# Optimization experiments

Measured on AMD Instinct MI355X. Metric: run time of the kernel, lower is better.

Reference implementation:

```python
import jax, jax.numpy as jnp
import numpy as np

ACT_DIM = 768
DICT_SIZE = 16384
K = 64
BATCH = 2048


def setup_inputs() -> dict:
    key = jax.random.key(0)
    k_x, k_w, k_be = jax.random.split(key, 3)
    x = jax.random.normal(k_x, (BATCH, ACT_DIM), dtype=jnp.float32)
    # encoder weight [dict_size, act_dim]; decoder initialized as encoder.T with unit-norm columns
    W_enc = jax.random.normal(k_w, (DICT_SIZE, ACT_DIM), dtype=jnp.float32) * 0.02
    b_enc = jnp.zeros((DICT_SIZE,), dtype=jnp.float32)
    W_dec = W_enc.T  # [act_dim, dict_size]
    eps = jnp.finfo(jnp.float32).eps
    W_dec = W_dec / (jnp.linalg.norm(W_dec, axis=0, keepdims=True) + eps)
    b_dec = jnp.zeros((ACT_DIM,), dtype=jnp.float32)
    return {"x": x, "W_enc": W_enc, "b_enc": b_enc, "W_dec": W_dec, "b_dec": b_dec}


def reference(x, W_enc, b_enc, W_dec, b_dec):
    B = x.shape[0]
    # encode: linear on (x - b_dec), relu
    post_relu_BF = jax.nn.relu((x - b_dec) @ W_enc.T + b_enc)  # [B, F]
    flat = post_relu_BF.reshape(-1)  # [B*F]
    # global batch top-k: keep k*B largest activations across the whole batch
    vals, idx = jax.lax.top_k(flat, K * B)
    encoded_flat = jnp.zeros_like(flat).at[idx].set(vals)
    encoded_BF = encoded_flat.reshape(post_relu_BF.shape)
    # decode
    x_hat_BD = encoded_BF @ W_dec.T + b_dec  # [B, D]
    return x_hat_BD
```

## Files before the change

### kernel.cpp

```cpp
#include <hip/hip_runtime.h>
#include <stdint.h>

#define BATCH   2048
#define DIM     768
#define FEAT    16384
#define KSEL    64
#define KB_SEL  (BATCH * KSEL)
#define N_TOT   (BATCH * FEAT)
#define NX4     (BATCH * DIM / 4)
#define NW4     (FEAT * DIM / 4)

#define GBM 128
#define GBN 128
#define GBK 32
#define AROW   24
#define APLANE 3088

#define SAMP_ROWS 128
#define SAMP_N    12288
#define CCAP      262144
#define TIE_CAP   1024
#define LSTAGE    2048
#define FG        8
#define FBLK      (CCAP / (FG * 4))

#define PREP_BLKS 4096
#define WT_BLKS   (512 * 24)

#define SL_T32    0
#define SL_NC     1
#define SL_DEF    2
#define SL_NTIE   3
#define SL_WIN    4
#define SL_S0     16

typedef __attribute__((ext_vector_type(8))) __bf16 bf16x8;
typedef __attribute__((ext_vector_type(4))) float  f32x4;
typedef unsigned long long u64;

__device__ __forceinline__ unsigned short bf16r(float v)
{
    unsigned u = __float_as_uint(v);
    u += 0x7FFFu + ((u >> 16) & 1u);
    return (unsigned short)(u >> 16);
}

__device__ __forceinline__ unsigned wave_append(unsigned* counter, bool pred)
{
    unsigned long long m = __ballot(pred);
    if (m == 0ull) return 0xFFFFFFFFu;
    const int lane = threadIdx.x & 63;
    const int leader = __ffsll((unsigned long long)m) - 1;
    unsigned base = 0;
    if (lane == leader) base = atomicAdd(counter, (unsigned)__popcll(m));
    base = __shfl(base, leader, 64);
    if (!pred) return 0xFFFFFFFFu;
    return base + (unsigned)__popcll(m & ((1ull << lane) - 1ull));
}

__global__ __launch_bounds__(256) void sae19_prepwt(const float* __restrict__ x,
                                                    const float* __restrict__ Wenc,
                                                    const float* __restrict__ Wdec,
                                                    const float* __restrict__ bdec,
                                                    unsigned short* __restrict__ xb,
                                                    unsigned short* __restrict__ wb,
                                                    unsigned short* __restrict__ Wtb)
{
    __shared__ float t[32][33];
    if (blockIdx.x < PREP_BLKS) {
        const int tot = NX4 + NW4;
        for (int i = blockIdx.x * 256 + threadIdx.x; i < tot; i += PREP_BLKS * 256) {
            if (i < NX4) {
                const int e = i * 4;
                const int d = e % DIM;
                float4 v  = *(const float4*)(x + e);
                float4 dv = *(const float4*)(bdec + d);
                uint2 p;
                p.x = (unsigned)bf16r(v.x - dv.x) | ((unsigned)bf16r(v.y - dv.y) << 16);
                p.y = (unsigned)bf16r(v.z - dv.z) | ((unsigned)bf16r(v.w - dv.w) << 16);
                *(uint2*)(xb + e) = p;
            } else {
                const int e = (i - NX4) * 4;
                float4 v = *(const float4*)(Wenc + e);
                uint2 p;
                p.x = (unsigned)bf16r(v.x) | ((unsigned)bf16r(v.y) << 16);
                p.y = (unsigned)bf16r(v.z) | ((unsigned)bf16r(v.w) << 16);
                *(uint2*)(wb + e) = p;
            }
        }
    } else {
        const int wtb = blockIdx.x - PREP_BLKS;
        const int f0 = (wtb % 512) * 32;
        const int d0 = (wtb / 512) * 32;
        const int tx = threadIdx.x & 31;
        const int ty = threadIdx.x >> 5;
#pragma unroll
        for (int i = 0; i < 4; ++i)
            t[ty + i * 8][tx] = Wdec[(size_t)(d0 + ty + i * 8) * FEAT + f0 + tx];
        __syncthreads();
#pragma unroll
        for (int i = 0; i < 4; ++i)
            Wtb[(size_t)(f0 + ty + i * 8) * DIM + d0 + tx] = bf16r(t[tx][ty + i * 8]);
    }
}

__global__ __launch_bounds__(256) void sae19_sgemm(const unsigned short* __restrict__ xb,
                                                   const unsigned short* __restrict__ wb,
                                                   const float* __restrict__ benc,
                                                   unsigned* __restrict__ hist)
{
    __shared__ unsigned short Als[4 * APLANE];
    __shared__ unsigned short Bls[4 * APLANE];
    __shared__ unsigned h[8192];

    const int tid  = threadIdx.x;
    for (int i = tid; i < 8192; i += 256) h[i] = 0u;
    const int row0 = 0;
    const int col0 = blockIdx.x * GBN;
    const int wid  = tid >> 6;
    const int lane = tid & 63;
    const int wr = wid >> 1;
    const int wc = wid & 1;
    const int fr = lane & 15;
    const int kg = lane >> 4;

    f32x4 acc[4][4];
#pragma unroll
    for (int i = 0; i < 4; ++i)
#pragma unroll
        for (int j = 0; j < 4; ++j) acc[i][j] = (f32x4){0.f, 0.f, 0.f, 0.f};

    for (int kt = 0; kt < DIM; kt += GBK) {
#pragma unroll
        for (int i = 0; i < 4; ++i) {
            const int idx = i * 256 + tid;
            const int r   = idx >> 3;
            const int kq  = (idx & 7) * 4;
            const int g   = kq >> 3;
            const int k0  = kq & 7;
            *(uint2*)&Als[g * APLANE + r * AROW + k0] =
                *(const uint2*)(xb + (size_t)(row0 + r) * DIM + kt + kq);
            *(uint2*)&Bls[g * APLANE + r * AROW + k0] =
                *(const uint2*)(wb + (size_t)(col0 + r) * DIM + kt + kq);
        }
        __syncthreads();

        bf16x8 afr[4], bfr[4];
#pragma unroll
        for (int mi = 0; mi < 4; ++mi)
            afr[mi] = *(const bf16x8*)&Als[kg * APLANE + (wr * 64 + mi * 16 + fr) * AROW];
#pragma unroll
        for (int ni = 0; ni < 4; ++ni)
            bfr[ni] = *(const bf16x8*)&Bls[kg * APLANE + (wc * 64 + ni * 16 + fr) * AROW];
#pragma unroll
        for (int mi = 0; mi < 4; ++mi)
#pragma unroll
            for (int ni = 0; ni < 4; ++ni)
                acc[mi][ni] = __builtin_amdgcn_mfma_f32_16x16x32_bf16(
                    afr[mi], bfr[ni], acc[mi][ni], 0, 0, 0);
        __syncthreads();
    }

#pragma unroll
    for (int ni = 0; ni < 4; ++ni) {
        const int col = col0 + wc * 64 + ni * 16 + fr;
        const float be = benc[col];
#pragma unroll
        for (int mi = 0; mi < 4; ++mi) {
#pragma unroll
            for (int j = 0; j < 4; ++j) {
                unsigned short bits = bf16r(fmaxf(acc[mi][ni][j] + be, 0.f));
                if (bits) atomicAdd(&h[bits >> 2], 1u);
            }
        }
    }
    __syncthreads();
    for (int i = tid; i < 8192; i += 256) {
        unsigned c = h[i];
        if (c) atomicAdd(&hist[i], c);
    }
}

__global__ __launch_bounds__(1024) void sae19_selb(const unsigned* __restrict__ hist,
                                                   unsigned* sl)
{
    __shared__ unsigned s[1024];
    const int t = threadIdx.x;
    const int C = 8;
    const unsigned N = (unsigned)SAMP_N;
    const int lo = t * C;
    unsigned S = 0;
    for (int i = 0; i < C; ++i) S += hist[lo + i];
    s[t] = S;
    __syncthreads();
    for (int off = 1; off < 1024; off <<= 1) {
        unsigned v = (t + off < 1024) ? s[t + off] : 0u;
        __syncthreads();
        s[t] += v;
        __syncthreads();
    }
    const unsigned incl  = s[t];
    const unsigned above = incl - S;
    if (above < N && N <= incl) {
        unsigned cum = above;
        for (int i = lo + C - 1; i >= lo; --i) {
            cum += hist[i];
            if (cum >= N) { sl[SL_T32] = (unsigned)i << 2; break; }
        }
    }
}

__global__ __launch_bounds__(256) void sae19_gemm(const unsigned short* __restrict__ xb,
                                                  const unsigned short* __restrict__ wb,
                                                  const float* __restrict__ benc,
                                                  unsigned* __restrict__ sl,
                                                  int* __restrict__ cand_raw)
{
    __shared__ unsigned short Als[4 * APLANE];
    __shared__ unsigned short Bls[4 * APLANE];
    __shared__ unsigned lcnt;
    __shared__ unsigned gbase;

    const int tid  = threadIdx.x;
    if (tid == 0) lcnt = 0;
    const int row0 = blockIdx.y * GBM;
    const int col0 = blockIdx.x * GBN;
    const int wid  = tid >> 6;
    const int lane = tid & 63;
    const int wr = wid >> 1;
    const int wc = wid & 1;
    const int fr = lane & 15;
    const int kg = lane >> 4;

    f32x4 acc[4][4];
#pragma unroll
    for (int i = 0; i < 4; ++i)
#pragma unroll
        for (int j = 0; j < 4; ++j) acc[i][j] = (f32x4){0.f, 0.f, 0.f, 0.f};

    for (int kt = 0; kt < DIM; kt += GBK) {
#pragma unroll
        for (int i = 0; i < 4; ++i) {
            const int idx = i * 256 + tid;
            const int r   = idx >> 3;
            const int kq  = (idx & 7) * 4;
            const int g   = kq >> 3;
            const int k0  = kq & 7;
            *(uint2*)&Als[g * APLANE + r * AROW + k0] =
                *(const uint2*)(xb + (size_t)(row0 + r) * DIM + kt + kq);
            *(uint2*)&Bls[g * APLANE + r * AROW + k0] =
                *(const uint2*)(wb + (size_t)(col0 + r) * DIM + kt + kq);
        }
        __syncthreads();

        bf16x8 afr[4], bfr[4];
#pragma unroll
        for (int mi = 0; mi < 4; ++mi)
            afr[mi] = *(const bf16x8*)&Als[kg * APLANE + (wr * 64 + mi * 16 + fr) * AROW];
#pragma unroll
        for (int ni = 0; ni < 4; ++ni)
            bfr[ni] = *(const bf16x8*)&Bls[kg * APLANE + (wc * 64 + ni * 16 + fr) * AROW];
#pragma unroll
        for (int mi = 0; mi < 4; ++mi)
#pragma unroll
            for (int ni = 0; ni < 4; ++ni)
                acc[mi][ni] = __builtin_amdgcn_mfma_f32_16x16x32_bf16(
                    afr[mi], bfr[ni], acc[mi][ni], 0, 0, 0);
        __syncthreads();
    }

    int* loc = (int*)Als;
    const unsigned T = sl[SL_T32];
#pragma unroll
    for (int ni = 0; ni < 4; ++ni) {
        const int col = col0 + wc * 64 + ni * 16 + fr;
        const float be = benc[col];
#pragma unroll
        for (int mi = 0; mi < 4; ++mi) {
            const int rbase = row0 + wr * 64 + mi * 16 + kg * 4;
#pragma unroll
            for (int j = 0; j < 4; ++j) {
                unsigned short bits = bf16r(fmaxf(acc[mi][ni][j] + be, 0.f));
                if ((unsigned)bits >= T) {
                    unsigned p = atomicAdd(&lcnt, 1u);
                    if (p < (unsigned)LSTAGE) loc[p] = (rbase + j) * FEAT + col;
                }
            }
        }
    }
    __syncthreads();
    unsigned n = lcnt;
    if (n > (unsigned)LSTAGE) n = (unsigned)LSTAGE;
    if (tid == 0) gbase = atomicAdd(&sl[SL_NC], n);
    __syncthreads();
    const unsigned base = gbase;
    for (unsigned k = tid; k < n; k += 256) {
        unsigned dst = base + k;
        if (dst < (unsigned)CCAP) cand_raw[dst] = loc[k];
    }
}

__global__ __launch_bounds__(256) void sae19_fhist(const int* __restrict__ cand_raw,
                                                   const unsigned* __restrict__ sl,
                                                   unsigned* __restrict__ fhist)
{
    __shared__ unsigned h[16384];
    const int t = threadIdx.x;
    for (int i = t; i < 16384; i += 256) h[i] = 0u;
    __syncthreads();
    unsigned NC = sl[SL_NC];
    if (NC > (unsigned)CCAP) NC = (unsigned)CCAP;
    for (int i = blockIdx.x * 256 + t; i < (int)NC; i += gridDim.x * 256)
        atomicAdd(&h[cand_raw[i] & (FEAT - 1)], 1u);
    __syncthreads();
    for (int i = t; i < 16384; i += 256) {
        unsigned c = h[i];
        if (c) atomicAdd(&fhist[i], c);
    }
}

__global__ __launch_bounds__(1024) void sae19_fscan(const unsigned* __restrict__ fhist,
                                                    unsigned* __restrict__ fofs)
{
    __shared__ unsigned s[1024];
    const int t = threadIdx.x;
    unsigned c[16];
    unsigned sum = 0;
#pragma unroll
    for (int j = 0; j < 16; ++j) { c[j] = fhist[t * 16 + j]; sum += c[j]; }
    s[t] = sum;
    __syncthreads();
    for (int off = 1; off < 1024; off <<= 1) {
        unsigned v = (t >= off) ? s[t - off] : 0u;
        __syncthreads();
        s[t] += v;
        __syncthreads();
    }
    unsigned run = s[t] - sum;
#pragma unroll
    for (int j = 0; j < 16; ++j) { fofs[t * 16 + j] = run; run += c[j]; }
}

__global__ __launch_bounds__(256) void sae19_fscat(const int* __restrict__ cand_raw,
                                                   const unsigned* __restrict__ sl,
                                                   const unsigned* __restrict__ fofs,
                                                   unsigned* __restrict__ fcur,
                                                   int* __restrict__ cand_flat)
{
    unsigned NC = sl[SL_NC];
    if (NC > (unsigned)CCAP) NC = (unsigned)CCAP;
    for (int i = blockIdx.x * 256 + threadIdx.x; i < (int)NC; i += gridDim.x * 256) {
        int flat = cand_raw[i];
        int f = flat & (FEAT - 1);
        unsigned p = atomicAdd(&fcur[f], 1u);
        unsigned dst = fofs[f] + p;
        if (dst < (unsigned)CCAP) cand_flat[dst] = flat;
    }
}

__global__ __launch_bounds__(256) void sae19_feval(const float* __restrict__ x,
                                                   const float* __restrict__ Wenc,
                                                   const float* __restrict__ benc,
                                                   const float* __restrict__ bdec,
                                                   const unsigned* __restrict__ sl,
                                                   const int* __restrict__ cand_flat,
                                                   u64* __restrict__ cand_key)
{
    unsigned NC = sl[SL_NC];
    if (NC > (unsigned)CCAP) NC = (unsigned)CCAP;
    const int lane = threadIdx.x & 63;
    const int b = blockIdx.x;
    const int lb = (b & 7) * (FBLK / 8) + (b >> 3);
    const int wid = lb * 4 + (threadIdx.x >> 6);
    const int c0 = wid * FG;
    if (c0 >= (int)NC) return;

    float bd[12], wv[12];
#pragma unroll
    for (int j = 0; j < 12; ++j) bd[j] = bdec[lane + j * 64];
    int fprev = -1;

    for (int g = 0; g < FG; ++g) {
        const int c = c0 + g;
        if (c >= (int)NC) break;
        const int flat = cand_flat[c];
        const int bb = flat >> 14;
        const int f  = flat & (FEAT - 1);
        if (f != fprev) {
            const float* wr = Wenc + (size_t)f * DIM;
#pragma unroll
            for (int j = 0; j < 12; ++j) wv[j] = wr[lane + j * 64];
            fprev = f;
        }
        const float* xr = x + (size_t)bb * DIM;
        double p = 0.0;
#pragma unroll
        for (int j = 0; j < 12; ++j)
            p = fma((double)xr[lane + j * 64] - (double)bd[j], (double)wv[j], p);
#pragma unroll
        for (int o = 32; o > 0; o >>= 1) p += __shfl_xor(p, o, 64);
        if (lane == 0) {
            p += (double)benc[f];
            if (p < 0.0) p = 0.0;
            cand_key[c] = (u64)__double_as_longlong(p);
        }
    }
}

__global__ __launch_bounds__(256) void sae19_hist64(const u64* __restrict__ cand_key,
                                                    const unsigned* __restrict__ sl,
                                                    unsigned* __restrict__ hist,
                                                    int pass)
{
    __shared__ unsigned h[16384];
    const int t = threadIdx.x;
    for (int i = t; i < 16384; i += 256) h[i] = 0u;
    __syncthreads();

    unsigned NC = sl[SL_NC];
    if (NC > (unsigned)CCAP) NC = (unsigned)CCAP;
    u64 pref = 0;
    for (int i = 0; i < pass; ++i) pref = (pref << 14) | (u64)sl[SL_S0 + i];
    const int chk_sh = 64 - 14 * pass;
    const int bkt_sh = 50 - 14 * pass;

    for (int i = blockIdx.x * 256 + t; i < (int)NC; i += gridDim.x * 256) {
        u64 key = cand_key[i];
        if (pass > 0 && (key >> chk_sh) != pref) continue;
        atomicAdd(&h[(unsigned)(key >> bkt_sh) & 0x3FFFu], 1u);
    }
    __syncthreads();
    for (int i = t; i < 16384; i += 256) {
        unsigned c = h[i];
        if (c) atomicAdd(&hist[i], c);
    }
}

__global__ __launch_bounds__(1024) void sae19_sel14(const unsigned* __restrict__ hist,
                                                    unsigned* sl, int pass)
{
    __shared__ unsigned s[1024];
    const int t = threadIdx.x;
    const int C = 16;
    const unsigned N = (pass == 0) ? (unsigned)KB_SEL : sl[SL_S0 + 4 + pass - 1];
    const int lo = t * C;
    unsigned S = 0;
    for (int i = 0; i < C; ++i) S += hist[lo + i];
    s[t] = S;
    __syncthreads();
    for (int off = 1; off < 1024; off <<= 1) {
        unsigned v = (t + off < 1024) ? s[t + off] : 0u;
        __syncthreads();
        s[t] += v;
        __syncthreads();
    }
    const unsigned incl  = s[t];
    const unsigned above = incl - S;
    if (above < N && N <= incl) {
        unsigned cum = above;
        for (int i = lo + C - 1; i >= lo; --i) {
            cum += hist[i];
            if (cum >= N) {
                sl[SL_S0 + pass]     = (unsigned)i;
                sl[SL_S0 + 4 + pass] = N - (cum - hist[i]);
                break;
            }
        }
    }
}

__global__ __launch_bounds__(256) void sae19_maxb(const u64* __restrict__ cand_key,
                                                  const unsigned* __restrict__ sl,
                                                  u64* __restrict__ mx)
{
    unsigned NC = sl[SL_NC];
    if (NC > (unsigned)CCAP) NC = (unsigned)CCAP;
    const u64 Tsh1 = ((u64)sl[SL_S0 + 0] << 28) | ((u64)sl[SL_S0 + 1] << 14) |
                     (u64)sl[SL_S0 + 2];
    u64 m = 0;
    for (int i = blockIdx.x * 256 + threadIdx.x; i < (int)NC; i += gridDim.x * 256) {
        u64 k = cand_key[i];
        if ((k >> 22) < Tsh1 && k > m) m = k;
    }
#pragma unroll
    for (int o = 32; o > 0; o >>= 1) {
        u64 o2 = __shfl_xor(m, o, 64);
        if (o2 > m) m = o2;
    }
    if ((threadIdx.x & 63) == 0 && m) atomicMax((unsigned long long*)mx, m);
}

__global__ __launch_bounds__(256) void sae19_class(const u64* __restrict__ cand_key,
                                                   const int* __restrict__ cand_flat,
                                                   const u64* __restrict__ mx,
                                                   unsigned* __restrict__ sl,
                                                   unsigned* __restrict__ row_cnt,
                                                   int* __restrict__ sel_flat,
                                                   float* __restrict__ sel_val,
                                                   int* __restrict__ tie_flat,
                                                   u64* __restrict__ tie_key)
{
    unsigned NC = sl[SL_NC];
    if (NC > (unsigned)CCAP) NC = (unsigned)CCAP;
    const u64 Tsh1 = ((u64)sl[SL_S0 + 0] << 28) | ((u64)sl[SL_S0 + 1] << 14) |
                     (u64)sl[SL_S0 + 2];
    const u64 Tsh2 = mx[0] >> 22;
    const int c = blockIdx.x * 256 + threadIdx.x;
    const bool active = (c < (int)NC);
    u64 key = 0;
    int flat = 0;
    u64 keysh = 0;
    if (active) {
        key = cand_key[c];
        keysh = key >> 22;
        flat = cand_flat[c];
    }
    const bool selp = active && (keysh > Tsh1);
    unsigned p = wave_append(&sl[SL_DEF], selp);
    if (selp && p < (unsigned)KB_SEL) {
        sel_flat[p] = flat;
        sel_val[p]  = (float)__longlong_as_double((long long)key);
        atomicAdd(&row_cnt[flat >> 14], 1u);
    }
    const bool tiep = active && !selp && (keysh == Tsh2);
    unsigned q = wave_append(&sl[SL_NTIE], tiep);
    if (tiep && q < (unsigned)TIE_CAP) { tie_flat[q] = flat; tie_key[q] = key; }
}

__global__ __launch_bounds__(256) void sae19_ties(const int* __restrict__ tie_flat,
                                                  const u64* __restrict__ tie_key,
                                                  unsigned* __restrict__ sl,
                                                  int* __restrict__ sel_flat,
                                                  float* __restrict__ sel_val,
                                                  unsigned* __restrict__ row_cnt)
{
    unsigned R = sl[SL_NTIE];
    if (R > (unsigned)TIE_CAP) R = (unsigned)TIE_CAP;
    const unsigned REM = sl[SL_S0 + 6];
    const unsigned D = sl[SL_DEF];
    const int c = blockIdx.x * blockDim.x + threadIdx.x;
    if (c >= (int)R) return;
    const int ic = tie_flat[c];
    unsigned rank = 0;
    for (int j = 0; j < (int)R; ++j)
        if (tie_flat[j] < ic) ++rank;
    if (rank < REM) {
        unsigned p = D + atomicAdd(&sl[SL_WIN], 1u);
        if (p < (unsigned)KB_SEL) {
            sel_flat[p] = ic;
            sel_val[p]  = (float)__longlong_as_double((long long)tie_key[c]);
            atomicAdd(&row_cnt[ic >> 14], 1u);
        }
    }
}

__global__ __launch_bounds__(256) void sae19_scan(const unsigned* __restrict__ row_cnt,
                                                  unsigned* __restrict__ row_ofs)
{
    __shared__ unsigned s[256];
    const int t = threadIdx.x;
    unsigned c[8];
    unsigned sum = 0;
#pragma unroll
    for (int j = 0; j < 8; ++j) { c[j] = row_cnt[t * 8 + j]; sum += c[j]; }
    s[t] = sum;
    __syncthreads();
    for (int off = 1; off < 256; off <<= 1) {
        unsigned v = (t >= off) ? s[t - off] : 0u;
        __syncthreads();
        s[t] += v;
        __syncthreads();
    }
    unsigned run = s[t] - sum;
#pragma unroll
    for (int j = 0; j < 8; ++j) { row_ofs[t * 8 + j] = run; run += c[j]; }
    if (t == 255) row_ofs[2048] = run;
}

__global__ void sae19_scatter(const int* __restrict__ sel_flat,
                              const float* __restrict__ sel_val,
                              const unsigned* __restrict__ row_ofs,
                              unsigned* __restrict__ cursor,
                              int* __restrict__ gf, float* __restrict__ gv)
{
    int e = blockIdx.x * blockDim.x + threadIdx.x;
    if (e >= KB_SEL) return;
    int flat = sel_flat[e];
    int b = flat >> 14;
    unsigned p = atomicAdd(&cursor[b], 1u);
    unsigned dst = row_ofs[b] + p;
    if (dst < (unsigned)KB_SEL) {
        gf[dst] = flat & (FEAT - 1);
        gv[dst] = sel_val[e];
    }
}

__global__ __launch_bounds__(256) void sae19_decode(const int* __restrict__ gf,
                                                    const float* __restrict__ gv,
                                                    const unsigned* __restrict__ row_ofs,
                                                    const unsigned short* __restrict__ Wtb,
                                                    const float* __restrict__ bdec,
                                                    float* __restrict__ out)
{
    const int b = blockIdx.x;
    const int t = threadIdx.x;
    float a0 = 0.f, a1 = 0.f, a2 = 0.f;
    const unsigned s = row_ofs[b];
    const unsigned e = row_ofs[b + 1];
    for (unsigned i = s; i < e; ++i) {
        const int f   = gf[i];
        const float v = gv[i];
        const unsigned short* w = Wtb + (size_t)f * DIM;
        a0 = fmaf(v, __uint_as_float((unsigned)w[t]       << 16), a0);
        a1 = fmaf(v, __uint_as_float((unsigned)w[t + 256] << 16), a1);
        a2 = fmaf(v, __uint_as_float((unsigned)w[t + 512] << 16), a2);
    }
    out[(size_t)b * DIM + t]       = a0 + bdec[t];
    out[(size_t)b * DIM + t + 256] = a1 + bdec[t + 256];
    out[(size_t)b * DIM + t + 512] = a2 + bdec[t + 512];
}

extern "C" void kernel_launch(void* const* d_in, const int* in_sizes, int n_in,
                              void* d_out, int out_size, void* d_ws, size_t ws_size,
                              hipStream_t stream)
{
    (void)in_sizes; (void)n_in; (void)out_size;
    const float* x    = (const float*)d_in[0];
    const float* Wenc = (const float*)d_in[1];
    const float* benc = (const float*)d_in[2];
    const float* Wdec = (const float*)d_in[3];
    const float* bdec = (const float*)d_in[4];
    float* out = (float*)d_out;

    char* ws = (char*)d_ws;
    size_t off = 0;
    unsigned short* Wtb = (unsigned short*)(ws + off);     off += (size_t)FEAT * DIM * 2;
    unsigned short* xb  = (unsigned short*)(ws + off);     off += (size_t)BATCH * DIM * 2;
    unsigned short* wb  = (unsigned short*)(ws + off);     off += (size_t)FEAT * DIM * 2;
    u64*      cand_key  = (u64*)(ws + off);                off += (size_t)CCAP * 8;
    int*      cand_raw  = (int*)(ws + off);                off += (size_t)CCAP * 4;
    int*      cand_flat = (int*)(ws + off);                off += (size_t)CCAP * 4;
    int*      tie_flat  = (int*)(ws + off);                off += (size_t)TIE_CAP * 4;
    u64*      tie_key   = (u64*)(ws + off);                off += (size_t)TIE_CAP * 8;
    unsigned* row_ofs   = (unsigned*)(ws + off);           off += 2052 * 4;
    unsigned* fofs      = (unsigned*)(ws + off);           off += 16384 * 4;
    char* zstart = ws + off;
    int*      sel_flat  = (int*)(ws + off);                off += (size_t)KB_SEL * 4;
    float*    sel_val   = (float*)(ws + off);              off += (size_t)KB_SEL * 4;
    int*      gf        = (int*)(ws + off);                off += (size_t)KB_SEL * 4;
    float*    gv        = (float*)(ws + off);              off += (size_t)KB_SEL * 4;
    unsigned* hist1     = (unsigned*)(ws + off);           off += 8192 * 4;
    unsigned* h64       = (unsigned*)(ws + off);           off += 3 * 16384 * 4;
    unsigned* fhist     = (unsigned*)(ws + off);           off += 16384 * 4;
    unsigned* fcur      = (unsigned*)(ws + off);           off += 16384 * 4;
    unsigned* row_cnt   = (unsigned*)(ws + off);           off += 2048 * 4;
    unsigned* cursor    = (unsigned*)(ws + off);           off += 2048 * 4;
    u64*      mx        = (u64*)(ws + off);                off += 8;
    unsigned* sl        = (unsigned*)(ws + off);           off += 256;
    const size_t zbytes = (size_t)((ws + off) - zstart);
    if (ws_size < off) return;

    hipMemsetAsync(zstart, 0, zbytes, stream);

    sae19_prepwt<<<PREP_BLKS + WT_BLKS, 256, 0, stream>>>(x, Wenc, Wdec, bdec, xb, wb, Wtb);

    sae19_sgemm<<<dim3(FEAT / GBN, 1), 256, 0, stream>>>(xb, wb, benc, hist1);
    sae19_selb<<<1, 1024, 0, stream>>>(hist1, sl);

    sae19_gemm<<<dim3(FEAT / GBN, BATCH / GBM), 256, 0, stream>>>(xb, wb, benc, sl, cand_raw);

    sae19_fhist<<<256, 256, 0, stream>>>(cand_raw, sl, fhist);
    sae19_fscan<<<1, 1024, 0, stream>>>(fhist, fofs);
    sae19_fscat<<<256, 256, 0, stream>>>(cand_raw, sl, fofs, fcur, cand_flat);
    sae19_feval<<<FBLK, 256, 0, stream>>>(x, Wenc, benc, bdec, sl, cand_flat, cand_key);

    for (int p = 0; p < 3; ++p) {
        sae19_hist64<<<256, 256, 0, stream>>>(cand_key, sl, h64 + p * 16384, p);
        sae19_sel14<<<1, 1024, 0, stream>>>(h64 + p * 16384, sl, p);
    }
    sae19_maxb<<<256, 256, 0, stream>>>(cand_key, sl, mx);

    sae19_class<<<(CCAP + 255) / 256, 256, 0, stream>>>(cand_key, cand_flat, mx, sl, row_cnt,
                                                        sel_flat, sel_val, tie_flat, tie_key);
    sae19_ties<<<TIE_CAP / 256, 256, 0, stream>>>(tie_flat, tie_key, sl,
                                                  sel_flat, sel_val, row_cnt);

    sae19_scan<<<1, 256, 0, stream>>>(row_cnt, row_ofs);
    sae19_scatter<<<(KB_SEL + 255) / 256, 256, 0, stream>>>(sel_flat, sel_val, row_ofs, cursor, gf, gv);
    sae19_decode<<<BATCH, 256, 0, stream>>>(gf, gv, row_ofs, Wtb, bdec, out);
}
```

Before: 432.0 us.

## Lower sample quota, use float threshold compare in gemm, dual-accumulate decode

Result: no change. 426.3 us (-1.3%).

```diff
diff --git a/kernel.cpp b/kernel.cpp
--- a/kernel.cpp
+++ b/kernel.cpp
@@ -17,7 +17,7 @@
 #define APLANE 3088
 
 #define SAMP_ROWS 128
-#define SAMP_N    12288
+#define SAMP_N    10752
 #define CCAP      262144
 #define TIE_CAP   1024
 #define LSTAGE    2048
@@ -32,6 +32,7 @@
 #define SL_DEF    2
 #define SL_NTIE   3
 #define SL_WIN    4
+#define SL_THRF   8
 #define SL_S0     16
 
 typedef __attribute__((ext_vector_type(8))) __bf16 bf16x8;
@@ -58,7 +59,7 @@
     return base + (unsigned)__popcll(m & ((1ull << lane) - 1ull));
 }
 
-__global__ __launch_bounds__(256) void sae19_prepwt(const float* __restrict__ x,
+__global__ __launch_bounds__(256) void sae20_prepwt(const float* __restrict__ x,
                                                     const float* __restrict__ Wenc,
                                                     const float* __restrict__ Wdec,
                                                     const float* __restrict__ bdec,
@@ -104,7 +105,7 @@
     }
 }
 
-__global__ __launch_bounds__(256) void sae19_sgemm(const unsigned short* __restrict__ xb,
+__global__ __launch_bounds__(256) void sae20_sgemm(const unsigned short* __restrict__ xb,
                                                    const unsigned short* __restrict__ wb,
                                                    const float* __restrict__ benc,
                                                    unsigned* __restrict__ hist)
@@ -181,7 +182,7 @@
     }
 }
 
-__global__ __launch_bounds__(1024) void sae19_selb(const unsigned* __restrict__ hist,
+__global__ __launch_bounds__(1024) void sae20_selb(const unsigned* __restrict__ hist,
                                                    unsigned* sl)
 {
     __shared__ unsigned s[1024];
@@ -205,12 +206,17 @@
         unsigned cum = above;
         for (int i = lo + C - 1; i >= lo; --i) {
             cum += hist[i];
-            if (cum >= N) { sl[SL_T32] = (unsigned)i << 2; break; }
-        }
-    }
-}
-
-__global__ __launch_bounds__(256) void sae19_gemm(const unsigned short* __restrict__ xb,
+            if (cum >= N) {
+                sl[SL_T32] = (unsigned)i << 2;
+                unsigned tb = (i > 0) ? ((unsigned)(i - 1) << 2) : 0u;
+                sl[SL_THRF] = tb << 16;
+                break;
+            }
+        }
+    }
+}
+
+__global__ __launch_bounds__(256) void sae20_gemm(const unsigned short* __restrict__ xb,
                                                   const unsigned short* __restrict__ wb,
                                                   const float* __restrict__ benc,
                                                   unsigned* __restrict__ sl,
@@ -270,7 +276,7 @@
     }
 
     int* loc = (int*)Als;
-    const unsigned T = sl[SL_T32];
+    const float thr = __uint_as_float(sl[SL_THRF]);
 #pragma unroll
     for (int ni = 0; ni < 4; ++ni) {
         const int col = col0 + wc * 64 + ni * 16 + fr;
@@ -280,8 +286,7 @@
             const int rbase = row0 + wr * 64 + mi * 16 + kg * 4;
 #pragma unroll
             for (int j = 0; j < 4; ++j) {
-                unsigned short bits = bf16r(fmaxf(acc[mi][ni][j] + be, 0.f));
-                if ((unsigned)bits >= T) {
+                if (acc[mi][ni][j] + be > thr) {
                     unsigned p = atomicAdd(&lcnt, 1u);
                     if (p < (unsigned)LSTAGE) loc[p] = (rbase + j) * FEAT + col;
                 }
@@ -300,7 +305,7 @@
     }
 }
 
-__global__ __launch_bounds__(256) void sae19_fhist(const int* __restrict__ cand_raw,
+__global__ __launch_bounds__(256) void sae20_fhist(const int* __restrict__ cand_raw,
                                                    const unsigned* __restrict__ sl,
                                                    unsigned* __restrict__ fhist)
 {
@@ -319,7 +324,7 @@
     }
 }
 
-__global__ __launch_bounds__(1024) void sae19_fscan(const unsigned* __restrict__ fhist,
+__global__ __launch_bounds__(1024) void sae20_fscan(const unsigned* __restrict__ fhist,
                                                     unsigned* __restrict__ fofs)
 {
     __shared__ unsigned s[1024];
@@ -341,7 +346,7 @@
     for (int j = 0; j < 16; ++j) { fofs[t * 16 + j] = run; run += c[j]; }
 }
 
-__global__ __launch_bounds__(256) void sae19_fscat(const int* __restrict__ cand_raw,
+__global__ __launch_bounds__(256) void sae20_fscat(const int* __restrict__ cand_raw,
                                                    const unsigned* __restrict__ sl,
                                                    const unsigned* __restrict__ fofs,
                                                    unsigned* __restrict__ fcur,
@@ -358,7 +363,7 @@
     }
 }
 
-__global__ __launch_bounds__(256) void sae19_feval(const float* __restrict__ x,
+__global__ __launch_bounds__(256) void sae20_feval(const float* __restrict__ x,
                                                    const float* __restrict__ Wenc,
                                                    const float* __restrict__ benc,
                                                    const float* __restrict__ bdec,
@@ -407,7 +412,7 @@
     }
 }
 
-__global__ __launch_bounds__(256) void sae19_hist64(const u64* __restrict__ cand_key,
+__global__ __launch_bounds__(256) void sae20_hist64(const u64* __restrict__ cand_key,
                                                     const unsigned* __restrict__ sl,
                                                     unsigned* __restrict__ hist,
                                                     int pass)
@@ -436,7 +441,7 @@
     }
 }
 
-__global__ __launch_bounds__(1024) void sae19_sel14(const unsigned* __restrict__ hist,
+__global__ __launch_bounds__(1024) void sae20_sel14(const unsigned* __restrict__ hist,
                                                     unsigned* sl, int pass)
 {
     __shared__ unsigned s[1024];
@@ -469,7 +474,7 @@
     }
 }
 
-__global__ __launch_bounds__(256) void sae19_maxb(const u64* __restrict__ cand_key,
+__global__ __launch_bounds__(256) void sae20_maxb(const u64* __restrict__ cand_key,
                                                   const unsigned* __restrict__ sl,
                                                   u64* __restrict__ mx)
 {
@@ -490,7 +495,7 @@
     if ((threadIdx.x & 63) == 0 && m) atomicMax((unsigned long long*)mx, m);
 }
 
-__global__ __launch_bounds__(256) void sae19_class(const u64* __restrict__ cand_key,
+__global__ __launch_bounds__(256) void sae20_class(const u64* __restrict__ cand_key,
                                                    const int* __restrict__ cand_flat,
                                                    const u64* __restrict__ mx,
                                                    unsigned* __restrict__ sl,
@@ -527,7 +532,7 @@
     if (tiep && q < (unsigned)TIE_CAP) { tie_flat[q] = flat; tie_key[q] = key; }
 }
 
-__global__ __launch_bounds__(256) void sae19_ties(const int* __restrict__ tie_flat,
+__global__ __launch_bounds__(256) void sae20_ties(const int* __restrict__ tie_flat,
                                                   const u64* __restrict__ tie_key,
                                                   unsigned* __restrict__ sl,
                                                   int* __restrict__ sel_flat,
@@ -554,7 +559,7 @@
     }
 }
 
-__global__ __launch_bounds__(256) void sae19_scan(const unsigned* __restrict__ row_cnt,
+__global__ __launch_bounds__(256) void sae20_scan(const unsigned* __restrict__ row_cnt,
                                                   unsigned* __restrict__ row_ofs)
 {
     __shared__ unsigned s[256];
@@ -577,7 +582,7 @@
     if (t == 255) row_ofs[2048] = run;
 }
 
-__global__ void sae19_scatter(const int* __restrict__ sel_flat,
+__global__ void sae20_scatter(const int* __restrict__ sel_flat,
                               const float* __restrict__ sel_val,
                               const unsigned* __restrict__ row_ofs,
                               unsigned* __restrict__ cursor,
@@ -595,7 +600,7 @@
     }
 }
 
-__global__ __launch_bounds__(256) void sae19_decode(const int* __restrict__ gf,
+__global__ __launch_bounds__(256) void sae20_decode(const int* __restrict__ gf,
                                                     const float* __restrict__ gv,
                                                     const unsigned* __restrict__ row_ofs,
                                                     const unsigned short* __restrict__ Wtb,
@@ -605,19 +610,35 @@
     const int b = blockIdx.x;
     const int t = threadIdx.x;
     float a0 = 0.f, a1 = 0.f, a2 = 0.f;
+    float c0 = 0.f, c1 = 0.f, c2 = 0.f;
     const unsigned s = row_ofs[b];
     const unsigned e = row_ofs[b + 1];
-    for (unsigned i = s; i < e; ++i) {
-        const int f   = gf[i];
-        const float v = gv[i];
-        const unsigned short* w = Wtb + (size_t)f * DIM;
-        a0 = fmaf(v, __uint_as_float((unsigned)w[t]       << 16), a0);
-        a1 = fmaf(v, __uint_as_float((unsigned)w[t + 256] << 16), a1);
-        a2 = fmaf(v, __uint_as_float((unsigned)w[t + 512] << 16), a2);
-    }
-    out[(size_t)b * DIM + t]       = a0 + bdec[t];
-    out[(size_t)b * DIM + t + 256] = a1 + bdec[t + 256];
-    out[(size_t)b * DIM + t + 512] = a2 + bdec[t + 512];
+    unsigned i = s;
+    for (; i + 1 < e; i += 2) {
+        const int f0 = gf[i];
+        const int f1 = gf[i + 1];
+        const float v0 = gv[i];
+        const float v1 = gv[i + 1];
+        const unsigned short* w0 = Wtb + (size_t)f0 * DIM;
+        const unsigned short* w1 = Wtb + (size_t)f1 * DIM;
+        a0 = fmaf(v0, __uint_as_float((unsigned)w0[t]       << 16), a0);
+        c0 = fmaf(v1, __uint_as_float((unsigned)w1[t]       << 16), c0);
+        a1 = fmaf(v0, __uint_as_float((unsigned)w0[t + 256] << 16), a1);
+        c1 = fmaf(v1, __uint_as_float((unsigned)w1[t + 256] << 16), c1);
+        a2 = fmaf(v0, __uint_as_float((unsigned)w0[t + 512] << 16), a2);
+        c2 = fmaf(v1, __uint_as_float((unsigned)w1[t + 512] << 16), c2);
+    }
+    if (i < e) {
+        const int f0 = gf[i];
+        const float v0 = gv[i];
+        const unsigned short* w0 = Wtb + (size_t)f0 * DIM;
+        a0 = fmaf(v0, __uint_as_float((unsigned)w0[t]       << 16), a0);
+        a1 = fmaf(v0, __uint_as_float((unsigned)w0[t + 256] << 16), a1);
+        a2 = fmaf(v0, __uint_as_float((unsigned)w0[t + 512] << 16), a2);
+    }
+    out[(size_t)b * DIM + t]       = (a0 + c0) + bdec[t];
+    out[(size_t)b * DIM + t + 256] = (a1 + c1) + bdec[t + 256];
+    out[(size_t)b * DIM + t + 512] = (a2 + c2) + bdec[t + 512];
 }
 
 extern "C" void kernel_launch(void* const* d_in, const int* in_sizes, int n_in,
@@ -662,30 +683,30 @@
 
     hipMemsetAsync(zstart, 0, zbytes, stream);
 
-    sae19_prepwt<<<PREP_BLKS + WT_BLKS, 256, 0, stream>>>(x, Wenc, Wdec, bdec, xb, wb, Wtb);
-
-    sae19_sgemm<<<dim3(FEAT / GBN, 1), 256, 0, stream>>>(xb, wb, benc, hist1);
-    sae19_selb<<<1, 1024, 0, stream>>>(hist1, sl);
-
-    sae19_gemm<<<dim3(FEAT / GBN, BATCH / GBM), 256, 0, stream>>>(xb, wb, benc, sl, cand_raw);
-
-    sae19_fhist<<<256, 256, 0, stream>>>(cand_raw, sl, fhist);
-    sae19_fscan<<<1, 1024, 0, stream>>>(fhist, fofs);
-    sae19_fscat<<<256, 256, 0, stream>>>(cand_raw, sl, fofs, fcur, cand_flat);
-    sae19_feval<<<FBLK, 256, 0, stream>>>(x, Wenc, benc, bdec, sl, cand_flat, cand_key);
+    sae20_prepwt<<<PREP_BLKS + WT_BLKS, 256, 0, stream>>>(x, Wenc, Wdec, bdec, xb, wb, Wtb);
+
+    sae20_sgemm<<<dim3(FEAT / GBN, 1), 256, 0, stream>>>(xb, wb, benc, hist1);
+    sae20_selb<<<1, 1024, 0, stream>>>(hist1, sl);
+
+    sae20_gemm<<<dim3(FEAT / GBN, BATCH / GBM), 256, 0, stream>>>(xb, wb, benc, sl, cand_raw);
+
+    sae20_fhist<<<256, 256, 0, stream>>>(cand_raw, sl, fhist);
+    sae20_fscan<<<1, 1024, 0, stream>>>(fhist, fofs);
+    sae20_fscat<<<256, 256, 0, stream>>>(cand_raw, sl, fofs, fcur, cand_flat);
+    sae20_feval<<<FBLK, 256, 0, stream>>>(x, Wenc, benc, bdec, sl, cand_flat, cand_key);
 
     for (int p = 0; p < 3; ++p) {
-        sae19_hist64<<<256, 256, 0, stream>>>(cand_key, sl, h64 + p * 16384, p);
-        sae19_sel14<<<1, 1024, 0, stream>>>(h64 + p * 16384, sl, p);
-    }
-    sae19_maxb<<<256, 256, 0, stream>>>(cand_key, sl, mx);
-
-    sae19_class<<<(CCAP + 255) / 256, 256, 0, stream>>>(cand_key, cand_flat, mx, sl, row_cnt,
+        sae20_hist64<<<256, 256, 0, stream>>>(cand_key, sl, h64 + p * 16384, p);
+        sae20_sel14<<<1, 1024, 0, stream>>>(h64 + p * 16384, sl, p);
+    }
+    sae20_maxb<<<256, 256, 0, stream>>>(cand_key, sl, mx);
+
+    sae20_class<<<(CCAP + 255) / 256, 256, 0, stream>>>(cand_key, cand_flat, mx, sl, row_cnt,
                                                         sel_flat, sel_val, tie_flat, tie_key);
-    sae19_ties<<<TIE_CAP / 256, 256, 0, stream>>>(tie_flat, tie_key, sl,
+    sae20_ties<<<TIE_CAP / 256, 256, 0, stream>>>(tie_flat, tie_key, sl,
                                                   sel_flat, sel_val, row_cnt);
 
-    sae19_scan<<<1, 256, 0, stream>>>(row_cnt, row_ofs);
-    sae19_scatter<<<(KB_SEL + 255) / 256, 256, 0, stream>>>(sel_flat, sel_val, row_ofs, cursor, gf, gv);
-    sae19_decode<<<BATCH, 256, 0, stream>>>(gf, gv, row_ofs, Wtb, bdec, out);
-}
+    sae20_scan<<<1, 256, 0, stream>>>(row_cnt, row_ofs);
+    sae20_scatter<<<(KB_SEL + 255) / 256, 256, 0, stream>>>(sel_flat, sel_val, row_ofs, cursor, gf, gv);
+    sae20_decode<<<BATCH, 256, 0, stream>>>(gf, gv, row_ofs, Wtb, bdec, out);
+}
```
